# Kernel optimization log

Measured on AMD Instinct MI355X. Metric: run time of the kernel, lower is better.

Reference implementation:

```python
import jax, jax.numpy as jnp
import numpy as np
from jax import lax

EPS = 1e-5

def conv2d(x, w, b=None, stride=1, pad=1):
    y = lax.conv_general_dilated(x, w, (stride, stride), ((pad, pad), (pad, pad)),
                                 dimension_numbers=('NCHW', 'OIHW', 'NCHW'))
    if b is not None:
        y = y + b[None, :, None, None]
    return y

def dcn(x, w_off, b_off, w, b):
    # modulated deformable conv (DCNv2): k=3, stride=1, pad=1, deformable_groups=1
    B, C, H, W = x.shape
    K = 9
    om = conv2d(x, w_off, b_off)  # [B, 3K, H, W] -> y-offsets, x-offsets, mask logits
    off_y, off_x = om[:, :K], om[:, K:2 * K]
    mask = jax.nn.sigmoid(om[:, 2 * K:])
    ky, kx = jnp.meshgrid(jnp.arange(3) - 1, jnp.arange(3) - 1, indexing='ij')
    py = jnp.arange(H)[None, None, :, None] + ky.reshape(K)[None, :, None, None] + off_y  # [B,K,H,W]
    px = jnp.arange(W)[None, None, None, :] + kx.reshape(K)[None, :, None, None] + off_x
    x_flat = x.reshape(B, C, H * W)
    y0 = jnp.floor(py)
    x0 = jnp.floor(px)
    acc = jnp.zeros((B, C, K, H * W), x.dtype)
    for dy in (0.0, 1.0):  # 4 bilinear corners (fixed small loop)
        for dx in (0.0, 1.0):
            yi = y0 + dy
            xi = x0 + dx
            wgt = (1.0 - jnp.abs(py - yi)) * (1.0 - jnp.abs(px - xi))
            valid = (yi >= 0) & (yi < H) & (xi >= 0) & (xi < W)  # zero padding outside
            yc = jnp.clip(yi, 0, H - 1).astype(jnp.int32)
            xc = jnp.clip(xi, 0, W - 1).astype(jnp.int32)
            flat = (yc * W + xc).reshape(B, K, H * W)
            g = jnp.take_along_axis(x_flat[:, :, None, :], flat[:, None, :, :], axis=3)  # [B,C,K,HW]
            acc = acc + g * (wgt * valid).reshape(B, 1, K, H * W)
    acc = acc * mask.reshape(B, 1, K, H * W)
    out = jnp.einsum('bckp,ock->bop', acc, w.reshape(w.shape[0], C, K))
    return out.reshape(B, w.shape[0], H, W) + b[None, :, None, None]

def bn_relu(x, gamma, beta, mean, var):
    inv = gamma / jnp.sqrt(var + EPS)
    return jax.nn.relu(x * inv[None, :, None, None] + (beta - mean * inv)[None, :, None, None])

def up_depthwise(x, w_up, f):
    # ConvTranspose2d(o, o, 2f, stride=f, padding=f//2, groups=o, bias=False)
    k = 2 * f
    p = k - 1 - f // 2
    return lax.conv_general_dilated(x, w_up[:, :, ::-1, ::-1], (1, 1), ((p, p), (p, p)),
                                    lhs_dilation=(f, f),
                                    dimension_numbers=('NCHW', 'OIHW', 'NCHW'),
                                    feature_group_count=w_up.shape[0])

def setup_inputs():
    key = jax.random.key(0)
    ks = jax.random.split(key, 12)
    B, CI, CO, H, W = 4, 256, 128, 64, 64
    f32 = jnp.float32
    d = {}
    d['x'] = jax.random.normal(ks[0], (B, CI, H, W), f32)
    d['w_off1'] = jax.random.normal(ks[1], (27, CI, 3, 3), f32) * 0.01
    d['b_off1'] = jnp.zeros((27,), f32)
    d['w1'] = jax.random.normal(ks[2], (CO, CI, 3, 3), f32) * (1.0 / np.sqrt(CI * 9))
    d['b1'] = jnp.zeros((CO,), f32)
    d['g1'] = jnp.ones((CO,), f32)
    d['be1'] = jnp.zeros((CO,), f32)
    d['m1'] = jax.random.normal(ks[3], (CO,), f32) * 0.1
    d['v1'] = jax.random.uniform(ks[4], (CO,), f32, 0.5, 1.5)
    d['w_up'] = jax.random.normal(ks[5], (CO, 1, 4, 4), f32) * 0.25
    d['w_off2'] = jax.random.normal(ks[6], (27, CO, 3, 3), f32) * 0.01
    d['b_off2'] = jnp.zeros((27,), f32)
    d['w2'] = jax.random.normal(ks[7], (CO, CO, 3, 3), f32) * (1.0 / np.sqrt(CO * 9))
    d['b2'] = jnp.zeros((CO,), f32)
    d['g2'] = jnp.ones((CO,), f32)
    d['be2'] = jnp.zeros((CO,), f32)
    d['m2'] = jax.random.normal(ks[8], (CO,), f32) * 0.1
    d['v2'] = jax.random.uniform(ks[9], (CO,), f32, 0.5, 1.5)
    return d

def reference(x, w_off1, b_off1, w1, b1, g1, be1, m1, v1, w_up,
              w_off2, b_off2, w2, b2, g2, be2, m2, v2):
    y = bn_relu(dcn(x, w_off1, b_off1, w1, b1), g1, be1, m1, v1)   # proj: [B,128,64,64]
    y = up_depthwise(y, w_up, 2)                                    # up:   [B,128,128,128]
    y = bn_relu(dcn(y, w_off2, b_off2, w2, b2), g2, be2, m2, v2)   # node: [B,128,128,128]
    return y
```

## Files before the change

kernel.cpp:

```cpp
#include <hip/hip_runtime.h>
#include <hip/hip_bf16.h>
#include <cmath>


#define EPSV 1e-5f

typedef __attribute__((ext_vector_type(8))) short short8;
typedef __attribute__((ext_vector_type(4))) float f32x4;

__device__ __forceinline__ ushort f2bf(float f) {
    union { float f; uint u; } v; v.f = f;
    const uint r = v.u + 0x7fffu + ((v.u >> 16) & 1u);
    return (ushort)(r >> 16);
}
__device__ __forceinline__ float bf2f(ushort h) {
    union { uint u; float f; } v; v.u = ((uint)h) << 16;
    return v.f;
}
__device__ __forceinline__ float2 ld2u(const float* p) {
    float2 v; __builtin_memcpy(&v, p, sizeof(float2)); return v;
}
__device__ __forceinline__ uint cvtpk_bf16(float a, float b) {
    uint r;
    asm("v_cvt_pk_bf16_f32 %0, %1, %2" : "=v"(r) : "v"(a), "v"(b));
    return r;
}

template <int KS>
__device__ __forceinline__ void pack_store8(
    const float* s, ushort* __restrict__ Shi, ushort* __restrict__ Slo,
    int pp, int j0)
{
    uint hw[4], lw[4];
#pragma unroll
    for (int q = 0; q < 4; ++q) {
        const float s0 = s[2 * q], s1 = s[2 * q + 1];
        const uint h = cvtpk_bf16(s0, s1);
        union { uint u; float f; } h0, h1;
        h0.u = h << 16;
        h1.u = h & 0xffff0000u;
        hw[q] = h;
        lw[q] = cvtpk_bf16(s0 - h0.f, s1 - h1.f);
    }
    uint4 hv; hv.x = hw[0]; hv.y = hw[1]; hv.z = hw[2]; hv.w = hw[3];
    uint4 lv; lv.x = lw[0]; lv.y = lw[1]; lv.z = lw[2]; lv.w = lw[3];
    *(uint4*)&Shi[pp * KS + j0] = hv;
    *(uint4*)&Slo[pp * KS + j0] = lv;
}

__global__ __launch_bounds__(256) void wsplit_perm_kernel(
    const float* __restrict__ w, ushort* __restrict__ hi,
    ushort* __restrict__ lo, int cin, int n)
{
    const int i = blockIdx.x * 256 + threadIdx.x;
    if (i >= n) return;
    const int cin9 = cin * 9;
    const int co = i / cin9;
    const int k  = i - co * cin9;
    const int ch = k >> 5;
    const int kq = (k & 31) >> 3;
    const int j  = k & 7;
    const int mt = co >> 4;
    const int lane = (co & 15) | (kq << 4);
    const size_t dst = ((size_t)(ch * 8 + mt) * 64 + lane) * 8 + j;
    const float f = w[i];
    const ushort h = f2bf(f);
    hi[dst] = h;
    lo[dst] = f2bf(f - bf2f(h));
}

__global__ __launch_bounds__(256) void wsplit_perm_conv_kernel(
    const float* __restrict__ w, ushort* __restrict__ hi,
    ushort* __restrict__ lo, int cin, int n)
{
    const int i = blockIdx.x * 256 + threadIdx.x;
    if (i >= n) return;
    const int cin9 = cin * 9;
    const int co = i / cin9;
    const int k  = i - co * cin9;
    const int ch = k >> 5;
    const int kq = (k & 31) >> 3;
    const int j  = k & 7;
    const int mt = co >> 4;
    const int lane = (co & 15) | (kq << 4);
    const size_t dst = ((size_t)(ch * 2 + mt) * 64 + lane) * 8 + j;
    const float f = (co < 27) ? w[(size_t)co * cin9 + k] : 0.f;
    const ushort h = f2bf(f);
    hi[dst] = h;
    lo[dst] = f2bf(f - bf2f(h));
}

template <int CIN, int HH, int WW, int POS, int KS>
__device__ __forceinline__ void conv_sample_chunk(
    const float* __restrict__ xb, const uint* __restrict__ toff,
    const float* __restrict__ twt, ushort* __restrict__ Shi,
    ushort* __restrict__ Slo, int tt, int kbase)
{
    constexpr int HW = HH * WW;
    const int pp = tt & (POS - 1);
    const int j0 = (tt / POS) * 8;
    float s[8];
#pragma unroll
    for (int j = 0; j < 8; ++j) {
        const int kg = kbase + j0 + j;
        const int c  = (kg * 7282) >> 16;
        const int k9 = kg - c * 9;
        const int ei = k9 * POS + pp;
        s[j] = xb[(size_t)c * HW + toff[ei]] * twt[ei];
    }
    pack_store8<KS>(s, Shi, Slo, pp, j0);
}

template <int CIN, int HH, int WW, int POS, int KWAVES, int MINW>
__global__ __launch_bounds__((POS / 16) * KWAVES * 64, MINW) void conv_mfma_kernel(
    const float* __restrict__ in,
    const ushort* __restrict__ whi,
    const ushort* __restrict__ wlo,
    const float* __restrict__ bias,
    float* __restrict__ om)
{
    constexpr int HW   = HH * WW;
    constexpr int K    = CIN * 9;
    constexpr int NPQ  = POS / 16;
    constexpr int NT   = NPQ * KWAVES * 64;
    constexpr int KC   = 32;
    constexpr int KS   = 40;
    constexpr int NCHT = K / KC;
    constexpr int NCH  = NCHT / KWAVES;
    constexpr int SBUF = POS * KS;

    extern __shared__ __align__(16) char smem[];
    uint*   toff  = (uint*)smem;
    float*  twt   = (float*)(toff + 9 * POS);
    ushort* Sbase = (ushort*)(twt + 9 * POS);

    const int tid = threadIdx.x;
    const int nt  = HW / POS;
    const int cpx = gridDim.x >> 3;
    const int bid = (blockIdx.x & 7) * cpx + (blockIdx.x >> 3);
    const int b   = bid / nt;
    const int p0  = (bid - b * nt) * POS;

    for (int i = tid; i < 9 * POS; i += NT) {
        const int k9 = i / POS, pp = i - k9 * POS;
        const int p  = p0 + pp;
        const int yy = p / WW, xx = p - yy * WW;
        const int ky = (k9 * 11) >> 5, kx = k9 - ky * 3;
        const int iy = yy + ky - 1, ix = xx + kx - 1;
        const bool v = (iy >= 0) && (iy < HH) && (ix >= 0) && (ix < WW);
        const int cy = min(max(iy, 0), HH - 1);
        const int cx = min(max(ix, 0), WW - 1);
        toff[i] = (uint)(cy * WW + cx);
        twt[i]  = v ? 1.f : 0.f;
    }
    __syncthreads();

    const float* xb = in + (size_t)b * CIN * HW;
    const int lane = tid & 63;
    const int w    = tid >> 6;
    const int wq   = w & (NPQ - 1);
    const int kgid = w / NPQ;
    const int tt   = tid & (NPQ * 64 - 1);
    ushort* S00 = Sbase + kgid * (4 * SBUF);

    f32x4 acc[2];
    acc[0] = (f32x4){0.f, 0.f, 0.f, 0.f};
    acc[1] = (f32x4){0.f, 0.f, 0.f, 0.f};
    const int mrow = lane & 15;
    const int kq   = lane >> 4;

    conv_sample_chunk<CIN, HH, WW, POS, KS>(xb, toff, twt, S00, S00 + SBUF,
                                            tt, kgid * NCH * KC);
    __syncthreads();

    for (int ch = 0; ch < NCH; ++ch) {
        const int cur = ch & 1;
        ushort* Sc = S00 + (cur * 2) * SBUF;
        const int boff = (wq * 16 + mrow) * KS + kq * 8;
        const short8 bh = *(const short8*)&Sc[boff];
        const short8 bl = *(const short8*)&Sc[SBUF + boff];
        if (ch + 1 < NCH) {
            ushort* Sn = S00 + ((cur ^ 1) * 2) * SBUF;
            conv_sample_chunk<CIN, HH, WW, POS, KS>(xb, toff, twt,
                                                    Sn, Sn + SBUF, tt,
                                                    (kgid * NCH + ch + 1) * KC);
        }
        const size_t abase = (size_t)((kgid * NCH + ch) * 2) * 512;
        __builtin_amdgcn_s_setprio(1);
#pragma unroll
        for (int mt = 0; mt < 2; ++mt) {
            const size_t ao = abase + (size_t)((mt * 64 + lane) * 8);
            const short8 ah = *(const short8*)(whi + ao);
            const short8 al = *(const short8*)(wlo + ao);
            acc[mt] = __builtin_amdgcn_mfma_f32_16x16x32_bf16(al, bh, acc[mt], 0, 0, 0);
            acc[mt] = __builtin_amdgcn_mfma_f32_16x16x32_bf16(ah, bl, acc[mt], 0, 0, 0);
            acc[mt] = __builtin_amdgcn_mfma_f32_16x16x32_bf16(ah, bh, acc[mt], 0, 0, 0);
        }
        __builtin_amdgcn_s_setprio(0);
        __syncthreads();
    }

    const int pcolb = wq * 16 + mrow;
    constexpr int RS = POS + 1;
    constexpr int SL = 32 * RS;
    float* red = (float*)Sbase;

    if constexpr (KWAVES == 4) {
        if (kgid >= 2) {
#pragma unroll
            for (int mt = 0; mt < 2; ++mt)
#pragma unroll
                for (int r = 0; r < 4; ++r) {
                    const int co = mt * 16 + kq * 4 + r;
                    red[(kgid - 2) * SL + co * RS + pcolb] = acc[mt][r];
                }
        }
        __syncthreads();
        if (kgid < 2) {
#pragma unroll
            for (int mt = 0; mt < 2; ++mt)
#pragma unroll
                for (int r = 0; r < 4; ++r) {
                    const int co = mt * 16 + kq * 4 + r;
                    acc[mt][r] += red[kgid * SL + co * RS + pcolb];
                }
        }
        __syncthreads();
        if (kgid == 1) {
#pragma unroll
            for (int mt = 0; mt < 2; ++mt)
#pragma unroll
                for (int r = 0; r < 4; ++r) {
                    const int co = mt * 16 + kq * 4 + r;
                    red[co * RS + pcolb] = acc[mt][r];
                }
        }
        __syncthreads();
        if (kgid == 0) {
#pragma unroll
            for (int mt = 0; mt < 2; ++mt)
#pragma unroll
                for (int r = 0; r < 4; ++r) {
                    const int co = mt * 16 + kq * 4 + r;
                    acc[mt][r] += red[co * RS + pcolb];
                }
        }
    } else if constexpr (KWAVES == 2) {
        if (kgid == 1) {
#pragma unroll
            for (int mt = 0; mt < 2; ++mt)
#pragma unroll
                for (int r = 0; r < 4; ++r) {
                    const int co = mt * 16 + kq * 4 + r;
                    red[co * RS + pcolb] = acc[mt][r];
                }
        }
        __syncthreads();
        if (kgid == 0) {
#pragma unroll
            for (int mt = 0; mt < 2; ++mt)
#pragma unroll
                for (int r = 0; r < 4; ++r) {
                    const int co = mt * 16 + kq * 4 + r;
                    acc[mt][r] += red[co * RS + pcolb];
                }
        }
    }

    if (kgid == 0) {
        float* ob = om + (size_t)b * 27 * HW + p0 + pcolb;
#pragma unroll
        for (int mt = 0; mt < 2; ++mt)
#pragma unroll
            for (int r = 0; r < 4; ++r) {
                const int co = mt * 16 + kq * 4 + r;
                if (co < 27)
                    ob[(size_t)co * HW] = acc[mt][r] + bias[co];
            }
    }
}

template <int CIN, int HH, int WW, int POS>
__device__ __forceinline__ void sample_issue(
    const float* __restrict__ xb, const uint* __restrict__ eoff2,
    float2* v0, float2* v1, int tt, int kbase)
{
    constexpr int HW = HH * WW;
    const int pp = tt & (POS - 1);
    const int j0 = (tt / POS) * 8;
#pragma unroll
    for (int j = 0; j < 8; ++j) {
        const int kg = kbase + j0 + j;
        const int c  = (kg * 7282) >> 16;
        const int k9 = kg - c * 9;
        const uint e = eoff2[k9 * POS + pp];
        const float* chp = xb + (size_t)c * HW;
        v0[j] = ld2u(chp + (e & 0xffffu));
        v1[j] = ld2u(chp + (e >> 16));
    }
}

template <int CIN, int HH, int WW, int POS, int KS>
__device__ __forceinline__ void sample_finish(
    const float4* __restrict__ ewt, const float2* v0, const float2* v1,
    ushort* __restrict__ Shi, ushort* __restrict__ Slo, int tt, int kbase)
{
    const int pp = tt & (POS - 1);
    const int j0 = (tt / POS) * 8;
    float s[8];
#pragma unroll
    for (int j = 0; j < 8; ++j) {
        const int kg = kbase + j0 + j;
        const int c  = (kg * 7282) >> 16;
        const int k9 = kg - c * 9;
        const float4 wv = ewt[k9 * POS + pp];
        s[j] = v0[j].x * wv.x + v0[j].y * wv.y
             + v1[j].x * wv.z + v1[j].y * wv.w;
    }
    pack_store8<KS>(s, Shi, Slo, pp, j0);
}

template <int CIN, int HH, int WW, int POS, int KS>
__device__ __forceinline__ void sample_chunk(
    const float* __restrict__ xb, const uint* __restrict__ eoff2,
    const float4* __restrict__ ewt, ushort* __restrict__ Shi,
    ushort* __restrict__ Slo, int tt, int kbase)
{
    float2 v0[8], v1[8];
    sample_issue<CIN, HH, WW, POS>(xb, eoff2, v0, v1, tt, kbase);
    sample_finish<CIN, HH, WW, POS, KS>(ewt, v0, v1, Shi, Slo, tt, kbase);
}

template <int CIN, int HH, int WW, int POS, int KWAVES, int MINW,
          bool ASTAGE, bool OMS>
__global__ __launch_bounds__((POS / 16) * KWAVES * 64, MINW) void dcn_mfma_kernel(
    const float* __restrict__ xin,
    const float* __restrict__ om,
    const float* __restrict__ omB,
    const ushort* __restrict__ whi,
    const ushort* __restrict__ wlo,
    const float* __restrict__ bias,
    const float* __restrict__ gam, const float* __restrict__ bet,
    const float* __restrict__ mu,  const float* __restrict__ var,
    float* __restrict__ out)
{
    constexpr int HW   = HH * WW;
    constexpr int K    = CIN * 9;
    constexpr int NPQ  = POS / 16;
    constexpr int NT   = NPQ * KWAVES * 64;
    constexpr int KC   = 32;
    constexpr int KS   = 40;
    constexpr int NCHT = K / KC;
    constexpr int NCH  = NCHT / KWAVES;
    constexpr int SBUF = POS * KS;
    constexpr int ABN  = ASTAGE ? 8192 : 0;
    constexpr int SN   = ASTAGE ? 2 * SBUF : KWAVES * 4 * SBUF;

    extern __shared__ __align__(16) char smem[];
    uint*    eoff2 = (uint*)smem;
    float4*  ewt   = (float4*)(eoff2 + 9 * POS);
    float*   invp  = (float*)(ewt + 9 * POS);
    float*   shp   = invp + 128;
    ushort*  Abuf  = (ushort*)(shp + 128);
    ushort*  Sbase = Abuf + ABN;
    (void)SN;

    const int tid = threadIdx.x;
    const int nt  = HW / POS;
    const int cpx = gridDim.x >> 3;
    const int bid = (blockIdx.x & 7) * cpx + (blockIdx.x >> 3);
    const int b   = bid / nt;
    const int p0  = (bid - b * nt) * POS;

    const float* omb  = om + (size_t)b * 27 * HW;
    const float* ombB = OMS ? (omB + (size_t)b * 27 * HW) : nullptr;
    for (int i = tid; i < 9 * POS; i += NT) {
        const int k9 = i / POS, pp = i - k9 * POS;
        const int p  = p0 + pp;
        const int yy = p / WW;
        const int xx = p - yy * WW;
        float oy = omb[(size_t)k9 * HW + p];
        float ox = omb[(size_t)(9 + k9) * HW + p];
        float mv = omb[(size_t)(18 + k9) * HW + p];
        if constexpr (OMS) {
            oy += ombB[(size_t)k9 * HW + p];
            ox += ombB[(size_t)(9 + k9) * HW + p];
            mv += ombB[(size_t)(18 + k9) * HW + p];
        }
        const float m  = 1.0f / (1.0f + expf(-mv));
        const int ky = (k9 * 11) >> 5;
        const int kx = k9 - ky * 3;
        const float py = (float)(yy + ky - 1) + oy;
        const float px = (float)(xx + kx - 1) + ox;
        const float y0f = floorf(py), x0f = floorf(px);
        const int   y0  = (int)y0f,  x0 = (int)x0f;
        const int by0 = min(max(y0, 0), HH - 1);
        const int by1 = min(max(y0 + 1, 0), HH - 1);
        const int bx  = min(max(x0, 0), WW - 2);
        const float wy1 = py - y0f, wx1 = px - x0f;
        const float fy0 = (y0 >= 0  && y0 < HH)     ? (1.f - wy1) * m : 0.f;
        const float fy1 = (y0 >= -1 && y0 < HH - 1) ? wy1 * m         : 0.f;
        const float fx0v = 1.f - wx1, fx1v = wx1;
        float gx0 = 0.f, gx1 = 0.f;
        if (x0 >= 0 && x0 < WW)         { if (x0 == bx)     gx0 += fx0v; else gx1 += fx0v; }
        if (x0 + 1 >= 0 && x0 + 1 < WW) { if (x0 + 1 == bx) gx0 += fx1v; else gx1 += fx1v; }
        eoff2[i] = (uint)(by0 * WW + bx) | ((uint)(by1 * WW + bx) << 16);
        float4 wv; wv.x = fy0 * gx0; wv.y = fy0 * gx1;
                   wv.z = fy1 * gx0; wv.w = fy1 * gx1;
        ewt[i] = wv;
    }
    for (int i = tid; i < 128; i += NT) {
        const float iv = gam[i] * rsqrtf(var[i] + EPSV);
        invp[i] = iv;
        shp[i]  = bet[i] - mu[i] * iv + bias[i] * iv;
    }
    __syncthreads();

    const float* xb   = xin + (size_t)b * CIN * HW;
    const int lane = tid & 63;
    const int w    = tid >> 6;
    const int wq   = w & (NPQ - 1);
    const int kgid = w / NPQ;
    const int tt   = tid & (NPQ * 64 - 1);

    f32x4 acc[8];
#pragma unroll
    for (int mt = 0; mt < 8; ++mt) acc[mt] = (f32x4){0.f, 0.f, 0.f, 0.f};

    const int mrow = lane & 15;
    const int kq   = lane >> 4;

    if constexpr (ASTAGE) {
        ushort* Shi = Sbase;
        ushort* Slo = Sbase + SBUF;
        float2 v0[8], v1[8];
        sample_chunk<CIN, HH, WW, POS, KS>(xb, eoff2, ewt, Shi, Slo, tt, 0);
        {
#pragma unroll
            for (int t = 0; t < 1024 / NT; ++t) {
                const int u = tid + t * NT;
                const ushort* srcp = (u < 512)
                    ? (whi + (size_t)u * 8)
                    : (wlo + (size_t)(u - 512) * 8);
                *(short8*)&Abuf[(size_t)u * 8] = *(const short8*)srcp;
            }
        }
        if (NCH > 1)
            sample_issue<CIN, HH, WW, POS>(xb, eoff2, v0, v1, tt, KC);
        asm volatile("s_waitcnt lgkmcnt(0)" ::: "memory");
        __builtin_amdgcn_s_barrier();
        __builtin_amdgcn_sched_barrier(0);

        for (int ch = 0; ch < NCH; ++ch) {
            const int boff = (wq * 16 + mrow) * KS + kq * 8;
            const short8 bh = *(const short8*)&Shi[boff];
            const short8 bl = *(const short8*)&Slo[boff];
            __builtin_amdgcn_s_setprio(1);
#pragma unroll
            for (int mt = 0; mt < 8; ++mt) {
                const int au = (mt * 64 + lane) * 8;
                const short8 ah = *(const short8*)&Abuf[au];
                const short8 al = *(const short8*)&Abuf[4096 + au];
                acc[mt] = __builtin_amdgcn_mfma_f32_16x16x32_bf16(al, bh, acc[mt], 0, 0, 0);
                acc[mt] = __builtin_amdgcn_mfma_f32_16x16x32_bf16(ah, bl, acc[mt], 0, 0, 0);
                acc[mt] = __builtin_amdgcn_mfma_f32_16x16x32_bf16(ah, bh, acc[mt], 0, 0, 0);
            }
            __builtin_amdgcn_s_setprio(0);
            if (ch + 1 < NCH) {
                asm volatile("s_waitcnt lgkmcnt(0)" ::: "memory");
                __builtin_amdgcn_s_barrier();
                __builtin_amdgcn_sched_barrier(0);
                const size_t wb = (size_t)(ch + 1) * 4096;
#pragma unroll
                for (int t = 0; t < 1024 / NT; ++t) {
                    const int u = tid + t * NT;
                    const ushort* srcp = (u < 512)
                        ? (whi + wb + (size_t)u * 8)
                        : (wlo + wb + (size_t)(u - 512) * 8);
                    *(short8*)&Abuf[(size_t)u * 8] = *(const short8*)srcp;
                }
                sample_finish<CIN, HH, WW, POS, KS>(ewt, v0, v1, Shi, Slo,
                                                    tt, (ch + 1) * KC);
                if (ch + 2 < NCH)
                    sample_issue<CIN, HH, WW, POS>(xb, eoff2, v0, v1, tt,
                                                   (ch + 2) * KC);
                asm volatile("s_waitcnt lgkmcnt(0)" ::: "memory");
                __builtin_amdgcn_s_barrier();
                __builtin_amdgcn_sched_barrier(0);
            }
        }
    } else {
        ushort* S00 = Sbase + kgid * (4 * SBUF);
        sample_chunk<CIN, HH, WW, POS, KS>(xb, eoff2, ewt, S00, S00 + SBUF,
                                           tt, kgid * NCH * KC);
        __syncthreads();

        for (int ch = 0; ch < NCH; ++ch) {
            const int cur = ch & 1;
            ushort* Sc = S00 + (cur * 2) * SBUF;
            const int boff = (wq * 16 + mrow) * KS + kq * 8;
            const short8 bh = *(const short8*)&Sc[boff];
            const short8 bl = *(const short8*)&Sc[SBUF + boff];
            if (ch + 1 < NCH) {
                ushort* Sn = S00 + ((cur ^ 1) * 2) * SBUF;
                sample_chunk<CIN, HH, WW, POS, KS>(xb, eoff2, ewt,
                                                   Sn, Sn + SBUF, tt,
                                                   (kgid * NCH + ch + 1) * KC);
            }
            const size_t abase = (size_t)((kgid * NCH + ch) * 8) * 512;
            __builtin_amdgcn_s_setprio(1);
#pragma unroll
            for (int mt = 0; mt < 8; ++mt) {
                const size_t ao = abase + (size_t)((mt * 64 + lane) * 8);
                const short8 ah = *(const short8*)(whi + ao);
                const short8 al = *(const short8*)(wlo + ao);
                acc[mt] = __builtin_amdgcn_mfma_f32_16x16x32_bf16(al, bh, acc[mt], 0, 0, 0);
                acc[mt] = __builtin_amdgcn_mfma_f32_16x16x32_bf16(ah, bl, acc[mt], 0, 0, 0);
                acc[mt] = __builtin_amdgcn_mfma_f32_16x16x32_bf16(ah, bh, acc[mt], 0, 0, 0);
            }
            __builtin_amdgcn_s_setprio(0);
            __syncthreads();
        }
    }

    const int pcolb = wq * 16 + mrow;
    constexpr int RS = POS + 1;
    constexpr int SL = 128 * RS;
    float* red = (float*)Sbase;

    if constexpr (KWAVES == 4) {
        if (kgid >= 2) {
#pragma unroll
            for (int mt = 0; mt < 8; ++mt)
#pragma unroll
                for (int r = 0; r < 4; ++r) {
                    const int co = mt * 16 + kq * 4 + r;
                    red[(kgid - 2) * SL + co * RS + pcolb] = acc[mt][r];
                }
        }
        __syncthreads();
        if (kgid < 2) {
#pragma unroll
            for (int mt = 0; mt < 8; ++mt)
#pragma unroll
                for (int r = 0; r < 4; ++r) {
                    const int co = mt * 16 + kq * 4 + r;
                    acc[mt][r] += red[kgid * SL + co * RS + pcolb];
                }
        }
        __syncthreads();
        if (kgid == 1) {
#pragma unroll
            for (int mt = 0; mt < 8; ++mt)
#pragma unroll
                for (int r = 0; r < 4; ++r) {
                    const int co = mt * 16 + kq * 4 + r;
                    red[co * RS + pcolb] = acc[mt][r];
                }
        }
        __syncthreads();
        if (kgid == 0) {
#pragma unroll
            for (int mt = 0; mt < 8; ++mt)
#pragma unroll
                for (int r = 0; r < 4; ++r) {
                    const int co = mt * 16 + kq * 4 + r;
                    acc[mt][r] += red[co * RS + pcolb];
                }
        }
    } else if constexpr (KWAVES == 2) {
        if (kgid == 1) {
#pragma unroll
            for (int mt = 0; mt < 8; ++mt)
#pragma unroll
                for (int r = 0; r < 4; ++r) {
                    const int co = mt * 16 + kq * 4 + r;
                    red[co * RS + pcolb] = acc[mt][r];
                }
        }
        __syncthreads();
        if (kgid == 0) {
#pragma unroll
            for (int mt = 0; mt < 8; ++mt)
#pragma unroll
                for (int r = 0; r < 4; ++r) {
                    const int co = mt * 16 + kq * 4 + r;
                    acc[mt][r] += red[co * RS + pcolb];
                }
        }
    }

    if (kgid == 0) {
        float* outb = out + (size_t)b * 128 * HW + p0 + pcolb;
#pragma unroll
        for (int mt = 0; mt < 8; ++mt)
#pragma unroll
            for (int r = 0; r < 4; ++r) {
                const int co = mt * 16 + kq * 4 + r;
                outb[(size_t)co * HW] = fmaxf(acc[mt][r] * invp[co] + shp[co], 0.f);
            }
    }
}

__global__ __launch_bounds__(256) void upsample_kernel(
    const float* __restrict__ y,
    const float* __restrict__ wup,
    float* __restrict__ out)
{
    const int idx = blockIdx.x * 256 + threadIdx.x;
    const int ox = idx & 127;
    const int oy = (idx >> 7) & 127;
    const int c  = (idx >> 14) & 127;
    const int b  = idx >> 21;

    const float* yc = y + (size_t)(b * 128 + c) * 4096;
    const float* wc = wup + c * 16;

    float acc = 0.f;
#pragma unroll
    for (int ky = 0; ky < 4; ++ky) {
        const int qy = oy + ky - 2;
        if (qy & 1) continue;
        const int iy = qy >> 1;
        if (iy < 0 || iy >= 64) continue;
#pragma unroll
        for (int kx = 0; kx < 4; ++kx) {
            const int qx = ox + kx - 2;
            if (qx & 1) continue;
            const int ix = qx >> 1;
            if (ix < 0 || ix >= 64) continue;
            acc += yc[iy * 64 + ix] * wc[(3 - ky) * 4 + (3 - kx)];
        }
    }
    out[idx] = acc;
}

extern "C" void kernel_launch(void* const* d_in, const int* in_sizes, int n_in,
                              void* d_out, int out_size, void* d_ws, size_t ws_size,
                              hipStream_t stream) {
    const float* x      = (const float*)d_in[0];
    const float* w_off1 = (const float*)d_in[1];
    const float* b_off1 = (const float*)d_in[2];
    const float* w1     = (const float*)d_in[3];
    const float* b1     = (const float*)d_in[4];
    const float* g1v    = (const float*)d_in[5];
    const float* be1    = (const float*)d_in[6];
    const float* m1     = (const float*)d_in[7];
    const float* v1     = (const float*)d_in[8];
    const float* w_up   = (const float*)d_in[9];
    const float* w_off2 = (const float*)d_in[10];
    const float* b_off2 = (const float*)d_in[11];
    const float* w2     = (const float*)d_in[12];
    const float* b2     = (const float*)d_in[13];
    const float* g2v    = (const float*)d_in[14];
    const float* be2    = (const float*)d_in[15];
    const float* m2     = (const float*)d_in[16];
    const float* v2     = (const float*)d_in[17];

    float* ws  = (float*)d_ws;
    float* om1 = ws;
    float* y1  = om1 + 442368;
    float* up  = y1 + 2097152;
    float* om2 = up + 8388608;
    float* outf = (float*)d_out;

    ushort* w1hi  = (ushort*)up;
    ushort* w1lo  = w1hi + 294912;
    ushort* wo1hi = w1lo + 294912;
    ushort* wo1lo = wo1hi + 73728;
    ushort* w2hi  = (ushort*)y1;
    ushort* w2lo  = w2hi + 147456;
    ushort* wo2hi = w2lo + 147456;
    ushort* wo2lo = wo2hi + 36864;

    wsplit_perm_kernel<<<(294912 + 255) / 256, 256, 0, stream>>>(
        w1, w1hi, w1lo, 256, 294912);
    wsplit_perm_conv_kernel<<<(73728 + 255) / 256, 256, 0, stream>>>(
        w_off1, wo1hi, wo1lo, 256, 73728);

    conv_mfma_kernel<256, 64, 64, 16, 4, 4>
        <<<1024, 256, 21632, stream>>>(x, wo1hi, wo1lo, b_off1, om1);

    dcn_mfma_kernel<256, 64, 64, 32, 4, 4, false, false>
        <<<4 * (4096 / 32), 512, 47744, stream>>>(
        x, om1, om1, w1hi, w1lo, b1, g1v, be1, m1, v1, y1);
    upsample_kernel<<<8388608 / 256, 256, 0, stream>>>(y1, w_up, up);

    wsplit_perm_kernel<<<(147456 + 255) / 256, 256, 0, stream>>>(
        w2, w2hi, w2lo, 128, 147456);
    wsplit_perm_conv_kernel<<<(36864 + 255) / 256, 256, 0, stream>>>(
        w_off2, wo2hi, wo2lo, 128, 36864);

    conv_mfma_kernel<128, 128, 128, 64, 1, 4>
        <<<1024, 256, 25088, stream>>>(up, wo2hi, wo2lo, b_off2, om2);

    dcn_mfma_kernel<128, 128, 128, 64, 1, 4, true, false>
        <<<4 * (16384 / 64), 256, 39168, stream>>>(
        up, om2, om2, w2hi, w2lo, b2, g2v, be2, m2, v2, outf);
}
```

Baseline: 382.2 us.

## Split MFMA tiles by output channels instead of positions across waves

Reassigns per-wave MFMA work so that each wave owns a subset of output-channel tiles across all position tiles, instead of one position tile across all channel tiles. Each wave now loads fewer A (weight) fragments and reuses them across several B fragments. The reduction and epilogue indexing are updated to match. This changes the LDS/global read balance between weights and sampled columns, and changes the output store pattern.

New measurement: 366.8 us. 4.0% less time.

```diff
diff --git a/kernel.cpp b/kernel.cpp
--- a/kernel.cpp
+++ b/kernel.cpp
@@ -354,7 +354,8 @@
     constexpr int NCH  = NCHT / KWAVES;
     constexpr int SBUF = POS * KS;
     constexpr int ABN  = ASTAGE ? 8192 : 0;
-    constexpr int SN   = ASTAGE ? 2 * SBUF : KWAVES * 4 * SBUF;
+    constexpr int MTW  = 8 / NPQ;
+    constexpr int NPT  = POS / 16;
 
     extern __shared__ __align__(16) char smem[];
     uint*    eoff2 = (uint*)smem;
@@ -363,7 +364,6 @@
     float*   shp   = invp + 128;
     ushort*  Abuf  = (ushort*)(shp + 128);
     ushort*  Sbase = Abuf + ABN;
-    (void)SN;
 
     const int tid = threadIdx.x;
     const int nt  = HW / POS;
@@ -419,9 +419,10 @@
     const float* xb   = xin + (size_t)b * CIN * HW;
     const int lane = tid & 63;
     const int w    = tid >> 6;
-    const int wq   = w & (NPQ - 1);
+    const int wm   = w & (NPQ - 1);
     const int kgid = w / NPQ;
     const int tt   = tid & (NPQ * 64 - 1);
+    const int m0   = wm * MTW;
 
     f32x4 acc[8];
 #pragma unroll
@@ -452,18 +453,27 @@
         __builtin_amdgcn_sched_barrier(0);
 
         for (int ch = 0; ch < NCH; ++ch) {
-            const int boff = (wq * 16 + mrow) * KS + kq * 8;
-            const short8 bh = *(const short8*)&Shi[boff];
-            const short8 bl = *(const short8*)&Slo[boff];
             __builtin_amdgcn_s_setprio(1);
-#pragma unroll
-            for (int mt = 0; mt < 8; ++mt) {
-                const int au = (mt * 64 + lane) * 8;
-                const short8 ah = *(const short8*)&Abuf[au];
-                const short8 al = *(const short8*)&Abuf[4096 + au];
-                acc[mt] = __builtin_amdgcn_mfma_f32_16x16x32_bf16(al, bh, acc[mt], 0, 0, 0);
-                acc[mt] = __builtin_amdgcn_mfma_f32_16x16x32_bf16(ah, bl, acc[mt], 0, 0, 0);
-                acc[mt] = __builtin_amdgcn_mfma_f32_16x16x32_bf16(ah, bh, acc[mt], 0, 0, 0);
+            short8 ahv[MTW], alv[MTW];
+#pragma unroll
+            for (int mt2 = 0; mt2 < MTW; ++mt2) {
+                const int au = ((m0 + mt2) * 64 + lane) * 8;
+                ahv[mt2] = *(const short8*)&Abuf[au];
+                alv[mt2] = *(const short8*)&Abuf[4096 + au];
+            }
+#pragma unroll
+            for (int pt = 0; pt < NPT; ++pt) {
+                const int boff = (pt * 16 + mrow) * KS + kq * 8;
+                const short8 bh = *(const short8*)&Shi[boff];
+                const short8 bl = *(const short8*)&Slo[boff];
+#pragma unroll
+                for (int mt2 = 0; mt2 < MTW; ++mt2) {
+                    f32x4 a = acc[mt2 * NPT + pt];
+                    a = __builtin_amdgcn_mfma_f32_16x16x32_bf16(alv[mt2], bh, a, 0, 0, 0);
+                    a = __builtin_amdgcn_mfma_f32_16x16x32_bf16(ahv[mt2], bl, a, 0, 0, 0);
+                    a = __builtin_amdgcn_mfma_f32_16x16x32_bf16(ahv[mt2], bh, a, 0, 0, 0);
+                    acc[mt2 * NPT + pt] = a;
+                }
             }
             __builtin_amdgcn_s_setprio(0);
             if (ch + 1 < NCH) {
@@ -498,9 +508,13 @@
         for (int ch = 0; ch < NCH; ++ch) {
             const int cur = ch & 1;
             ushort* Sc = S00 + (cur * 2) * SBUF;
-            const int boff = (wq * 16 + mrow) * KS + kq * 8;
-            const short8 bh = *(const short8*)&Sc[boff];
-            const short8 bl = *(const short8*)&Sc[SBUF + boff];
+            short8 bhv[NPT], blv[NPT];
+#pragma unroll
+            for (int pt = 0; pt < NPT; ++pt) {
+                const int boff = (pt * 16 + mrow) * KS + kq * 8;
+                bhv[pt] = *(const short8*)&Sc[boff];
+                blv[pt] = *(const short8*)&Sc[SBUF + boff];
+            }
             if (ch + 1 < NCH) {
                 ushort* Sn = S00 + ((cur ^ 1) * 2) * SBUF;
                 sample_chunk<CIN, HH, WW, POS, KS>(xb, eoff2, ewt,
@@ -510,20 +524,24 @@
             const size_t abase = (size_t)((kgid * NCH + ch) * 8) * 512;
             __builtin_amdgcn_s_setprio(1);
 #pragma unroll
-            for (int mt = 0; mt < 8; ++mt) {
-                const size_t ao = abase + (size_t)((mt * 64 + lane) * 8);
+            for (int mt2 = 0; mt2 < MTW; ++mt2) {
+                const size_t ao = abase + (size_t)(((m0 + mt2) * 64 + lane) * 8);
                 const short8 ah = *(const short8*)(whi + ao);
                 const short8 al = *(const short8*)(wlo + ao);
-                acc[mt] = __builtin_amdgcn_mfma_f32_16x16x32_bf16(al, bh, acc[mt], 0, 0, 0);
-                acc[mt] = __builtin_amdgcn_mfma_f32_16x16x32_bf16(ah, bl, acc[mt], 0, 0, 0);
-                acc[mt] = __builtin_amdgcn_mfma_f32_16x16x32_bf16(ah, bh, acc[mt], 0, 0, 0);
+#pragma unroll
+                for (int pt = 0; pt < NPT; ++pt) {
+                    f32x4 a = acc[mt2 * NPT + pt];
+                    a = __builtin_amdgcn_mfma_f32_16x16x32_bf16(al, bhv[pt], a, 0, 0, 0);
+                    a = __builtin_amdgcn_mfma_f32_16x16x32_bf16(ah, blv[pt], a, 0, 0, 0);
+                    a = __builtin_amdgcn_mfma_f32_16x16x32_bf16(ah, bhv[pt], a, 0, 0, 0);
+                    acc[mt2 * NPT + pt] = a;
+                }
             }
             __builtin_amdgcn_s_setprio(0);
             __syncthreads();
         }
     }
 
-    const int pcolb = wq * 16 + mrow;
     constexpr int RS = POS + 1;
     constexpr int SL = 128 * RS;
     float* red = (float*)Sbase;
@@ -531,74 +549,91 @@
     if constexpr (KWAVES == 4) {
         if (kgid >= 2) {
 #pragma unroll
-            for (int mt = 0; mt < 8; ++mt)
-#pragma unroll
-                for (int r = 0; r < 4; ++r) {
-                    const int co = mt * 16 + kq * 4 + r;
-                    red[(kgid - 2) * SL + co * RS + pcolb] = acc[mt][r];
-                }
+            for (int mt2 = 0; mt2 < MTW; ++mt2)
+#pragma unroll
+                for (int pt = 0; pt < NPT; ++pt)
+#pragma unroll
+                    for (int r = 0; r < 4; ++r) {
+                        const int co = (m0 + mt2) * 16 + kq * 4 + r;
+                        red[(kgid - 2) * SL + co * RS + pt * 16 + mrow] =
+                            acc[mt2 * NPT + pt][r];
+                    }
         }
         __syncthreads();
         if (kgid < 2) {
 #pragma unroll
-            for (int mt = 0; mt < 8; ++mt)
-#pragma unroll
-                for (int r = 0; r < 4; ++r) {
-                    const int co = mt * 16 + kq * 4 + r;
-                    acc[mt][r] += red[kgid * SL + co * RS + pcolb];
-                }
+            for (int mt2 = 0; mt2 < MTW; ++mt2)
+#pragma unroll
+                for (int pt = 0; pt < NPT; ++pt)
+#pragma unroll
+                    for (int r = 0; r < 4; ++r) {
+                        const int co = (m0 + mt2) * 16 + kq * 4 + r;
+                        acc[mt2 * NPT + pt][r] +=
+                            red[kgid * SL + co * RS + pt * 16 + mrow];
+                    }
         }
         __syncthreads();
         if (kgid == 1) {
 #pragma unroll
-            for (int mt = 0; mt < 8; ++mt)
-#pragma unroll
-                for (int r = 0; r < 4; ++r) {
-                    const int co = mt * 16 + kq * 4 + r;
-                    red[co * RS + pcolb] = acc[mt][r];
-                }
+            for (int mt2 = 0; mt2 < MTW; ++mt2)
+#pragma unroll
+                for (int pt = 0; pt < NPT; ++pt)
+#pragma unroll
+                    for (int r = 0; r < 4; ++r) {
+                        const int co = (m0 + mt2) * 16 + kq * 4 + r;
+                        red[co * RS + pt * 16 + mrow] = acc[mt2 * NPT + pt][r];
+                    }
         }
         __syncthreads();
         if (kgid == 0) {
 #pragma unroll
-            for (int mt = 0; mt < 8; ++mt)
-#pragma unroll
-                for (int r = 0; r < 4; ++r) {
-                    const int co = mt * 16 + kq * 4 + r;
-                    acc[mt][r] += red[co * RS + pcolb];
-                }
+            for (int mt2 = 0; mt2 < MTW; ++mt2)
+#pragma unroll
+                for (int pt = 0; pt < NPT; ++pt)
+#pragma unroll
+                    for (int r = 0; r < 4; ++r) {
+                        const int co = (m0 + mt2) * 16 + kq * 4 + r;
+                        acc[mt2 * NPT + pt][r] += red[co * RS + pt * 16 + mrow];
+                    }
         }
     } else if constexpr (KWAVES == 2) {
         if (kgid == 1) {
 #pragma unroll
-            for (int mt = 0; mt < 8; ++mt)
+            for (int mt2 = 0; mt2 < MTW; ++mt2)
+#pragma unroll
+                for (int pt = 0; pt < NPT; ++pt)
+#pragma unroll
+                    for (int r = 0; r < 4; ++r) {
+                        const int co = (m0 + mt2) * 16 + kq * 4 + r;
+                        red[co * RS + pt * 16 + mrow] = acc[mt2 * NPT + pt][r];
+                    }
+        }
+        __syncthreads();
+        if (kgid == 0) {
+#pragma unroll
+            for (int mt2 = 0; mt2 < MTW; ++mt2)
+#pragma unroll
+                for (int pt = 0; pt < NPT; ++pt)
+#pragma unroll
+                    for (int r = 0; r < 4; ++r) {
+                        const int co = (m0 + mt2) * 16 + kq * 4 + r;
+                        acc[mt2 * NPT + pt][r] += red[co * RS + pt * 16 + mrow];
+                    }
+        }
+    }
+
+    if (kgid == 0) {
+        float* outb = out + (size_t)b * 128 * HW + p0;
+#pragma unroll
+        for (int mt2 = 0; mt2 < MTW; ++mt2)
+#pragma unroll
+            for (int pt = 0; pt < NPT; ++pt)
 #pragma unroll
                 for (int r = 0; r < 4; ++r) {
-                    const int co = mt * 16 + kq * 4 + r;
-                    red[co * RS + pcolb] = acc[mt][r];
-                }
-        }
-        __syncthreads();
-        if (kgid == 0) {
-#pragma unroll
-            for (int mt = 0; mt < 8; ++mt)
-#pragma unroll
-                for (int r = 0; r < 4; ++r) {
-                    const int co = mt * 16 + kq * 4 + r;
-                    acc[mt][r] += red[co * RS + pcolb];
-                }
-        }
-    }
-
-    if (kgid == 0) {
-        float* outb = out + (size_t)b * 128 * HW + p0 + pcolb;
-#pragma unroll
-        for (int mt = 0; mt < 8; ++mt)
-#pragma unroll
-            for (int r = 0; r < 4; ++r) {
-                const int co = mt * 16 + kq * 4 + r;
-                outb[(size_t)co * HW] = fmaxf(acc[mt][r] * invp[co] + shp[co], 0.f);
-            }
+                    const int co = (m0 + mt2) * 16 + kq * 4 + r;
+                    outb[(size_t)co * HW + pt * 16 + mrow] =
+                        fmaxf(acc[mt2 * NPT + pt][r] * invp[co] + shp[co], 0.f);
+                }
     }
 }
 
```
